# Kernel tuning notes

Hardware: AMD Instinct MI355X
Metric: run time of the kernel (lower is better)

## Reference

```python
import jax, jax.numpy as jnp
import numpy as np
from jax import lax
import math

N_QUBITS = 10
N_LAYERS = 4
PI = jnp.float32(math.pi)


def _c(x):
    return x.astype(jnp.complex64)


def rx_mat(t):
    c = _c(jnp.cos(0.5 * t)); s = _c(jnp.sin(0.5 * t))
    return jnp.stack([jnp.stack([c, -1j * s]), jnp.stack([-1j * s, c])])


def ry_mat(t):
    c = _c(jnp.cos(0.5 * t)); s = _c(jnp.sin(0.5 * t))
    return jnp.stack([jnp.stack([c, -s]), jnp.stack([s, c])])


def rz_mat(t):
    e0 = jnp.exp(_c(jnp.zeros_like(t)) - 0.5j * _c(t))
    e1 = jnp.exp(0.5j * _c(t))
    z = jnp.zeros_like(e0)
    return jnp.stack([jnp.stack([e0, z]), jnp.stack([z, e1])])


def apply_1q(psi, U, q):
    # psi: (2,)*n complex, apply 2x2 U on axis q
    psi = jnp.moveaxis(psi, q, 0)
    psi = jnp.tensordot(U, psi, axes=(1, 0))
    return jnp.moveaxis(psi, 0, q)


def apply_cnot(psi, ctrl, tgt):
    psi = jnp.moveaxis(psi, (ctrl, tgt), (0, 1))
    a00, a01, a10, a11 = psi[0, 0], psi[0, 1], psi[1, 0], psi[1, 1]
    psi = jnp.stack([jnp.stack([a00, a01]), jnp.stack([a11, a10])])
    return jnp.moveaxis(psi, (0, 1), (ctrl, tgt))


def vqc(state, weights):
    # state: (D,) float32 angles; weights: (layers, n, 3)
    n, L = N_QUBITS, N_LAYERS
    D = state.shape[0]
    psi = jnp.full((2,) * n, 2.0 ** (-n / 2.0), dtype=jnp.complex64)  # H^n |0>
    for layer in range(L):
        for q in range(n):
            ang = state[(layer * n + q) % D]
            psi = apply_1q(psi, rx_mat(ang), q)
            psi = apply_1q(psi, ry_mat(ang), q)
            psi = apply_1q(psi, rz_mat(weights[layer, q, 0]), q)
            psi = apply_1q(psi, ry_mat(weights[layer, q, 1]), q)
            psi = apply_1q(psi, rz_mat(weights[layer, q, 2]), q)
        for q in range(n - 1):
            psi = apply_cnot(psi, q, q + 1)
        psi = apply_cnot(psi, n - 1, 0)
    probs = jnp.real(psi * jnp.conj(psi))  # (2,)*n
    zdiag = jnp.array([1.0, -1.0], dtype=jnp.float32)
    exps = [jnp.sum(probs * zdiag.reshape((1,) * q + (2,) + (1,) * (n - q - 1)))
            for q in range(n)]
    return jnp.stack(exps)  # (n,)


def lstm_forward(x, W_ih, W_hh, b_ih, b_hh):
    # x: [B,T,Din]; PyTorch gate order: i, f, g, o
    B, T, _ = x.shape
    H = W_hh.shape[1]
    b = b_ih + b_hh

    def step(carry, xt):
        h, c = carry
        gates = xt @ W_ih.T + h @ W_hh.T + b
        i, f, g, o = jnp.split(gates, 4, axis=-1)
        i = jax.nn.sigmoid(i); f = jax.nn.sigmoid(f)
        g = jnp.tanh(g); o = jax.nn.sigmoid(o)
        c = f * c + i * g
        h = o * jnp.tanh(c)
        return (h, c), h

    h0 = jnp.zeros((B, H), x.dtype)
    c0 = jnp.zeros((B, H), x.dtype)
    _, hs = lax.scan(step, (h0, c0), jnp.swapaxes(x, 0, 1))
    return jnp.swapaxes(hs, 0, 1)  # [B,T,H]


def _forward(s, lstm_s, W_ih, W_hh, b_ih, b_hh, proj_W, proj_b,
             in_proj_W, in_proj_b, out_proj_W, out_proj_b,
             qweights, W1, b1, W2, b2):
    hs = lstm_forward(lstm_s, W_ih, W_hh, b_ih, b_hh)      # [B,T,H]
    lstm_last = hs[:, -1, :]                               # [B,H]
    state_full = jnp.concatenate([lstm_last, s], axis=1)   # [B,E]
    lstm_proj = hs @ proj_W.T + proj_b                     # [B,T,E]
    E = proj_W.shape[0]
    Wq, Wk, Wv = in_proj_W[:E], in_proj_W[E:2 * E], in_proj_W[2 * E:]
    bq, bk, bv = in_proj_b[:E], in_proj_b[E:2 * E], in_proj_b[2 * E:]
    q = state_full @ Wq.T + bq                             # [B,E] (1 query token)
    k = lstm_proj @ Wk.T + bk                              # [B,T,E]
    v = lstm_proj @ Wv.T + bv
    scale = 1.0 / jnp.sqrt(jnp.float32(E))                 # num_heads=1 -> head_dim=E
    attn = jax.nn.softmax(jnp.einsum('be,bte->bt', q, k) * scale, axis=-1)
    ctx = jnp.einsum('bt,bte->be', attn, v)
    attn_out = ctx @ out_proj_W.T + out_proj_b             # [B,E]
    merged_state = jnp.concatenate([attn_out, s], axis=1)  # [B,E+F]
    state_norm = jnp.tanh(merged_state) * PI
    qfeat = jax.vmap(lambda st: vqc(st, qweights))(state_norm)  # [B,n]
    merged = jnp.concatenate([merged_state, qfeat], axis=1)
    x = jax.nn.relu(merged @ W1.T + b1)
    return x @ W2.T + b2


def setup_inputs() -> dict:
    key = jax.random.key(0)
    ks = jax.random.split(key, 16)
    B, T = 512, 256
    Din, H, F = 128, 256, 64
    E = H + F          # 320 = state_dim
    Dm = E + F         # 384 = merged_state dim
    n_l1, n_act = 512, 8

    def g(k, shape, std):
        return (std * jax.random.normal(k, shape)).astype(jnp.float32)

    return {
        's': jax.random.normal(ks[0], (B, F), jnp.float32),
        'lstm_s': jax.random.normal(ks[1], (B, T, Din), jnp.float32),
        'W_ih': g(ks[2], (4 * H, Din), 0.05),
        'W_hh': g(ks[3], (4 * H, H), 0.05),
        'b_ih': jnp.zeros((4 * H,), jnp.float32),
        'b_hh': jnp.zeros((4 * H,), jnp.float32),
        'proj_W': g(ks[4], (E, H), 0.05),
        'proj_b': 0.1 * jnp.ones((E,), jnp.float32),
        'in_proj_W': g(ks[5], (3 * E, E), 0.05),
        'in_proj_b': jnp.zeros((3 * E,), jnp.float32),
        'out_proj_W': g(ks[6], (E, E), 0.05),
        'out_proj_b': jnp.zeros((E,), jnp.float32),
        'qweights': jax.random.uniform(ks[7], (N_LAYERS, N_QUBITS, 3), jnp.float32, 0.0, 2.0 * math.pi),
        'W1': g(ks[8], (n_l1, Dm + N_QUBITS), 0.05),
        'b1': 0.1 * jnp.ones((n_l1,), jnp.float32),
        'W2': g(ks[9], (n_act, n_l1), 0.05),
        'b2': 0.1 * jnp.ones((n_act,), jnp.float32),
    }


def reference(s, lstm_s, W_ih, W_hh, b_ih, b_hh, proj_W, proj_b,
              in_proj_W, in_proj_b, out_proj_W, out_proj_b,
              qweights, W1, b1, W2, b2):
    return _forward(s, lstm_s, W_ih, W_hh, b_ih, b_hh, proj_W, proj_b,
                    in_proj_W, in_proj_b, out_proj_W, out_proj_b,
                    qweights, W1, b1, W2, b2)
```

## Files before the change

### kernel.cpp

```cpp
#include <hip/hip_runtime.h>
#include <hip/hip_bf16.h>
#include <math.h>

typedef unsigned int u32;
typedef unsigned long long u64;
typedef unsigned short u16;
typedef __attribute__((ext_vector_type(8))) short short8;
typedef __attribute__((ext_vector_type(4))) float f32x4;
typedef __attribute__((ext_vector_type(4))) int v4i;

#define PI_F 3.14159265358979f
#define B_   512
#define T_   256
#define DIN  128
#define H_   256
#define G4   1024
#define F_   64
#define E_   320
#define DM   384
#define NL1  512
#define NACT 8
#define KMLP 394

__device__ v4i llvm_amdgcn_raw_buffer_load_v4i32(v4i rsrc, int voffset,
                                                 int soffset, int aux)
    __asm("llvm.amdgcn.raw.buffer.load.v4i32");
__device__ void llvm_amdgcn_raw_buffer_store_i32(int vdata, v4i rsrc,
                                                 int voffset, int soffset,
                                                 int aux)
    __asm("llvm.amdgcn.raw.buffer.store.i32");

__device__ __forceinline__ v4i make_srd(const void* p) {
  v4i r;
  r.x = (int)(u32)(u64)p;
  r.y = (int)(u32)((u64)p >> 32);
  r.z = (int)0xFFFFFFFFu;
  r.w = 0x00020000;
  return r;
}

__device__ __forceinline__ float b2f(u16 h) {
  union { u32 u; float f; } v; v.u = ((u32)h) << 16; return v.f;
}
__device__ __forceinline__ u16 f2b(float f) {
  union { float f; u32 u; } v; v.f = f;
  u32 r = (v.u + 0x7FFFu + ((v.u >> 16) & 1u)) >> 16;
  return (u16)r;
}
__device__ __forceinline__ float sigf(float x) { return 1.0f / (1.0f + __expf(-x)); }
__device__ __forceinline__ float tanhfast(float x) { return 2.0f / (1.0f + __expf(-2.0f * x)) - 1.0f; }
__device__ __forceinline__ float2 cmul(float2 a, float2 b) {
  return make_float2(a.x * b.x - a.y * b.y, a.x * b.y + a.y * b.x);
}
__device__ __forceinline__ float2 cadd(float2 a, float2 b) {
  return make_float2(a.x + b.x, a.y + b.y);
}

__global__ void k_prep1(const float* __restrict__ lstm_s,
                        const float* __restrict__ W_ih,
                        const float* __restrict__ W_hh,
                        const float* __restrict__ b_ih,
                        const float* __restrict__ b_hh,
                        const float* __restrict__ ipw,
                        const float* __restrict__ ipb,
                        const float* __restrict__ projb,
                        const float* __restrict__ qw,
                        const float* __restrict__ W1,
                        u16* __restrict__ xbf,
                        u16* __restrict__ hs,
                        u16* __restrict__ Wg,
                        float* __restrict__ bb,
                        float* __restrict__ W1t,
                        float* __restrict__ uw,
                        float* __restrict__ bkp,
                        float* __restrict__ bvp,
                        u32* __restrict__ cnt) {
  const int bid = blockIdx.x;
  const int tid = threadIdx.x;
  if (bid < 8192) {
    u32 u = (u32)bid * 256u + tid;
    u32 c8 = u & 15u, b = (u >> 4) & 511u, t = u >> 13;
    const float* src = lstm_s + ((size_t)b * T_ + t) * DIN + c8 * 8;
    union { u16 h[8]; uint4 v; } tmp;
#pragma unroll
    for (int i = 0; i < 8; ++i) tmp.h[i] = f2b(src[i]);
    *(uint4*)(xbf + ((size_t)t * B_ + b) * DIN + c8 * 8) = tmp.v;
  } else if (bid < 8384) {
    u32 u = (u32)(bid - 8192) * 256u + tid;
    u32 c8 = u % 48u, r = u / 48u;
    const float* src = (c8 < 16) ? (W_ih + (size_t)r * DIN + c8 * 8)
                                 : (W_hh + (size_t)r * H_ + (c8 - 16) * 8);
    union { u16 h[8]; uint4 v; } tmp;
#pragma unroll
    for (int i = 0; i < 8; ++i) tmp.h[i] = f2b(src[i]);
    *(uint4*)(Wg + (size_t)r * 384 + c8 * 8) = tmp.v;
  } else if (bid < 8448) {
    u32 u = (u32)(bid - 8384) * 256u + tid;
    ((uint4*)hs)[u] = make_uint4(0, 0, 0, 0);
  } else if (bid < 9236) {
    u32 u = (u32)(bid - 8448) * 256u + tid;
    u32 k = u / 512u, nn = u % 512u;
    W1t[u] = W1[(size_t)nn * KMLP + k];
  } else if (bid == 9236) {
    for (int i = tid; i < 1024; i += 256) bb[i] = b_ih[i] + b_hh[i];
    for (int i = tid; i < 1024; i += 256) cnt[i] = 0u;
    if (tid < 40) {
      float w0 = qw[tid * 3 + 0], w1 = qw[tid * 3 + 1], w2 = qw[tid * 3 + 2];
      float c0 = cosf(0.5f * w0), s0 = sinf(0.5f * w0);
      float c1 = cosf(0.5f * w1), s1 = sinf(0.5f * w1);
      float c2 = cosf(0.5f * w2), s2 = sinf(0.5f * w2);
      float2 e0m = make_float2(c0, -s0), e0p = make_float2(c0, s0);
      float2 e2m = make_float2(c2, -s2), e2p = make_float2(c2, s2);
      float2 t00 = make_float2(c1 * e0m.x, c1 * e0m.y);
      float2 t01 = make_float2(-s1 * e0p.x, -s1 * e0p.y);
      float2 t10 = make_float2(s1 * e0m.x, s1 * e0m.y);
      float2 t11 = make_float2(c1 * e0p.x, c1 * e0p.y);
      float2 u00 = cmul(e2m, t00), u01 = cmul(e2m, t01);
      float2 u10 = cmul(e2p, t10), u11 = cmul(e2p, t11);
      float* o = uw + tid * 8;
      o[0] = u00.x; o[1] = u00.y; o[2] = u01.x; o[3] = u01.y;
      o[4] = u10.x; o[5] = u10.y; o[6] = u11.x; o[7] = u11.y;
    }
  } else if (bid <= 9238) {
    int o = (bid - 9237) * 256 + tid;
    if (o < E_) {
      float acc = ipb[E_ + o];
      for (int e = 0; e < E_; ++e) acc += ipw[(size_t)(E_ + o) * E_ + e] * projb[e];
      bkp[o] = acc;
    }
  } else {
    int o = (bid - 9239) * 256 + tid;
    if (o < E_) {
      float acc = ipb[2 * E_ + o];
      for (int e = 0; e < E_; ++e) acc += ipw[(size_t)(2 * E_ + o) * E_ + e] * projb[e];
      bvp[o] = acc;
    }
  }
}

__global__ void k_prep2(const float* __restrict__ ipw, const float* __restrict__ projW,
                        float* __restrict__ Wkp, float* __restrict__ Wvp) {
  int bid = blockIdx.x, tid = threadIdx.x;
  int o = (bid < 320) ? bid : (bid - 320);
  const float* wrow = ipw + (size_t)((bid < 320 ? E_ : 2 * E_) + o) * E_;
  float acc = 0.f;
  for (int e = 0; e < E_; ++e) acc += wrow[e] * projW[(size_t)e * H_ + tid];
  (bid < 320 ? Wkp : Wvp)[(size_t)o * H_ + tid] = acc;
}

__global__ void k_prep3(const float* __restrict__ ipw, const float* __restrict__ ipb,
                        const float* __restrict__ opw, const float* __restrict__ opb,
                        const float* __restrict__ Wkp, const float* __restrict__ Wvp,
                        const float* __restrict__ bkp, const float* __restrict__ bvp,
                        float* __restrict__ WuT, float* __restrict__ bu,
                        float* __restrict__ wd, float* __restrict__ ddp,
                        float* __restrict__ Wovt, float* __restrict__ bov) {
  int bid = blockIdx.x, tid = threadIdx.x;
  if (bid < 320) {
    int e = bid;
    float acc = 0.f;
    for (int o = 0; o < E_; ++o) acc += Wkp[(size_t)o * H_ + tid] * ipw[(size_t)o * E_ + e];
    WuT[(size_t)e * H_ + tid] = acc;
  } else if (bid < 576) {
    int jj = bid - 320;
    for (int i = tid; i < E_; i += 256) {
      float acc = 0.f;
      for (int o = 0; o < E_; ++o) acc += opw[(size_t)i * E_ + o] * Wvp[(size_t)o * H_ + jj];
      Wovt[(size_t)jj * E_ + i] = acc;
    }
  } else {
    {
      float acc = 0.f;
      for (int o = 0; o < E_; ++o) acc += Wkp[(size_t)o * H_ + tid] * ipb[o];
      bu[tid] = acc;
    }
    for (int idx = tid; idx < E_; idx += 256) {
      float a1 = 0.f, a2 = opb[idx];
      for (int o = 0; o < E_; ++o) {
        a1 += ipw[(size_t)o * E_ + idx] * bkp[o];
        a2 += opw[(size_t)idx * E_ + o] * bvp[o];
      }
      wd[idx] = a1; bov[idx] = a2;
    }
    if (tid == 0) {
      float acc = 0.f;
      for (int o = 0; o < E_; ++o) acc += ipb[o] * bkp[o];
      ddp[0] = acc;
    }
  }
}

struct LstmArgs {
  const u16* xbf; u16* hs; const u16* Wg; const float* bb; u32* cnt;
};

__launch_bounds__(256, 1)
__global__ void k_lstm(LstmArgs A) {
  const int g   = blockIdx.x & 7;
  const int n   = blockIdx.x >> 3;
  const int tid = threadIdx.x;
  const int wid = tid >> 6, lane = tid & 63;
  __shared__ __align__(16) u16 Wl[32 * 392];

  for (int idx = tid; idx < 32 * 48; idx += 256) {
    int ln = idx / 48, c8 = idx % 48;
    int gr = (ln >> 3) * 256 + n * 8 + (ln & 7);
    *(uint4*)&Wl[ln * 392 + c8 * 8] = *(const uint4*)&A.Wg[(size_t)gr * 384 + c8 * 8];
  }
  const int j  = lane & 7;
  const int gc = n * 8 + j;
  const float bbi = A.bb[gc], bbf2 = A.bb[256 + gc];
  const float bbg = A.bb[512 + gc], bbo = A.bb[768 + gc];

  const int quad = lane >> 4;
  const int mrow = lane & 15;
  const int brow = g * 64 + wid * 16 + mrow;
  const int erow0 = g * 64 + wid * 16 + quad * 4;
  const bool hi = (lane & 8) != 0;
  float crs[4] = {0.f, 0.f, 0.f, 0.f};
  u32* mycnt = A.cnt + g * 64;
  u32 target = 0;

  const v4i hs_srd = make_srd(A.hs);
  const int hvoff = (brow * H_ + quad * 8) * 2;

  uint4 xc0, xc1, xc2, xc3, xn0, xn1, xn2, xn3;
  {
    const u16* xb = A.xbf + ((size_t)0 * B_ + brow) * DIN + quad * 8;
    xc0 = *(const uint4*)(xb + 0);
    xc1 = *(const uint4*)(xb + 32);
    xc2 = *(const uint4*)(xb + 64);
    xc3 = *(const uint4*)(xb + 96);
  }
  __syncthreads();

  for (int t = 0; t < T_; ++t) {
    const int hsoff = t * (B_ * H_ * 2);
    uint4 h0 = __builtin_bit_cast(uint4, llvm_amdgcn_raw_buffer_load_v4i32(hs_srd, hvoff +   0, hsoff, 17));
    uint4 h1 = __builtin_bit_cast(uint4, llvm_amdgcn_raw_buffer_load_v4i32(hs_srd, hvoff +  64, hsoff, 17));
    uint4 h2 = __builtin_bit_cast(uint4, llvm_amdgcn_raw_buffer_load_v4i32(hs_srd, hvoff + 128, hsoff, 17));
    uint4 h3 = __builtin_bit_cast(uint4, llvm_amdgcn_raw_buffer_load_v4i32(hs_srd, hvoff + 192, hsoff, 17));
    uint4 h4 = __builtin_bit_cast(uint4, llvm_amdgcn_raw_buffer_load_v4i32(hs_srd, hvoff + 256, hsoff, 17));
    uint4 h5 = __builtin_bit_cast(uint4, llvm_amdgcn_raw_buffer_load_v4i32(hs_srd, hvoff + 320, hsoff, 17));
    uint4 h6 = __builtin_bit_cast(uint4, llvm_amdgcn_raw_buffer_load_v4i32(hs_srd, hvoff + 384, hsoff, 17));
    uint4 h7 = __builtin_bit_cast(uint4, llvm_amdgcn_raw_buffer_load_v4i32(hs_srd, hvoff + 448, hsoff, 17));
    {
      const int tn = (t + 1 < T_) ? (t + 1) : t;
      const u16* xb = A.xbf + ((size_t)tn * B_ + brow) * DIN + quad * 8;
      xn0 = *(const uint4*)(xb + 0);
      xn1 = *(const uint4*)(xb + 32);
      xn2 = *(const uint4*)(xb + 64);
      xn3 = *(const uint4*)(xb + 96);
    }

    f32x4 acc0 = {0.f, 0.f, 0.f, 0.f}, acc1 = {0.f, 0.f, 0.f, 0.f};
#define MMSTEP(AV, KOFF)                                                          \
    {                                                                             \
      short8 av  = __builtin_bit_cast(short8, AV);                                \
      short8 bv0 = __builtin_bit_cast(short8,                                     \
          *(const uint4*)&Wl[mrow * 392 + (KOFF) + quad * 8]);                    \
      short8 bv1 = __builtin_bit_cast(short8,                                     \
          *(const uint4*)&Wl[(16 + mrow) * 392 + (KOFF) + quad * 8]);             \
      acc0 = __builtin_amdgcn_mfma_f32_16x16x32_bf16(av, bv0, acc0, 0, 0, 0);     \
      acc1 = __builtin_amdgcn_mfma_f32_16x16x32_bf16(av, bv1, acc1, 0, 0, 0);     \
    }
    MMSTEP(xc0, 0)   MMSTEP(xc1, 32)  MMSTEP(xc2, 64)  MMSTEP(xc3, 96)
    MMSTEP(h0, 128)  MMSTEP(h1, 160)  MMSTEP(h2, 192)  MMSTEP(h3, 224)
    MMSTEP(h4, 256)  MMSTEP(h5, 288)  MMSTEP(h6, 320)  MMSTEP(h7, 352)
#undef MMSTEP

    const int hsoff_o = (t + 1) * (B_ * H_ * 2);
#pragma unroll
    for (int r = 0; r < 4; ++r) {
      float x0 = acc0[r], x1v = acc1[r];
      float y0 = __shfl_xor(x0, 8, 64);
      float y1 = __shfl_xor(x1v, 8, 64);
      float iv = (hi ? y0 : x0) + bbi;
      float fv = (hi ? x0 : y0) + bbf2;
      float gv = (hi ? y1 : x1v) + bbg;
      float ov = (hi ? x1v : y1) + bbo;
      float cc = sigf(fv) * crs[r] + sigf(iv) * tanhfast(gv);
      crs[r] = cc;
      float hh = sigf(ov) * tanhfast(cc);
      float hh2 = __shfl_xor(hh, 1, 64);
      if (!hi && ((j & 1) == 0)) {
        u32 pk = (u32)f2b(hh) | ((u32)f2b(hh2) << 16);
        llvm_amdgcn_raw_buffer_store_i32((int)pk, hs_srd,
                                         ((erow0 + r) * H_ + gc) * 2, hsoff_o, 17);
      }
    }
    target += 32;
    if (t != T_ - 1) {
      __syncthreads();
      if (tid == 0) {
        __hip_atomic_fetch_add(mycnt, 1u, __ATOMIC_RELAXED, __HIP_MEMORY_SCOPE_AGENT);
        int guard = 0;
        while (__hip_atomic_load(mycnt, __ATOMIC_RELAXED, __HIP_MEMORY_SCOPE_AGENT) < target) {
          __builtin_amdgcn_s_sleep(1);
          if (++guard > (1 << 24)) break;
        }
      }
      __syncthreads();
      xc0 = xn0; xc1 = xn1; xc2 = xn2; xc3 = xn3;
    }
  }
}

__global__ void k_u(const u16* __restrict__ hs, const float* __restrict__ s,
                    const float* __restrict__ WuT, const float* __restrict__ bu,
                    const float* __restrict__ wd, const float* __restrict__ ddp,
                    float* __restrict__ u, float* __restrict__ dvec) {
  int b = blockIdx.x, tid = threadIdx.x;
  __shared__ float z[E_];
  __shared__ float red[256];
  z[tid] = b2f(hs[((size_t)T_ * B_ + b) * H_ + tid]);
  if (tid < F_) z[H_ + tid] = s[(size_t)b * F_ + tid];
  __syncthreads();
  float acc = bu[tid];
  for (int e = 0; e < E_; ++e) acc += WuT[(size_t)e * H_ + tid] * z[e];
  u[(size_t)b * H_ + tid] = acc;
  float p = 0.f;
  for (int e = tid; e < E_; e += 256) p += wd[e] * z[e];
  red[tid] = p;
  __syncthreads();
  for (int s2 = 128; s2 > 0; s2 >>= 1) {
    if (tid < s2) red[tid] += red[tid + s2];
    __syncthreads();
  }
  if (tid == 0) dvec[b] = red[0] + ddp[0];
}

__global__ void k_aw(const u16* __restrict__ hs, const float* __restrict__ u,
                     const float* __restrict__ dvec, float* __restrict__ wv) {
  int b = blockIdx.x, tid = threadIdx.x;
  int wid = tid >> 6, lane = tid & 63;
  __shared__ float sc[T_];
  __shared__ float red[256];
  const float db = dvec[b];
  const float scale = 0.055901699437494745f;
  float4 ul = *(const float4*)&u[(size_t)b * H_ + lane * 4];
  for (int tt = 0; tt < 64; ++tt) {
    int t = wid * 64 + tt;
    u32 rw0 = ((const u32*)(hs + ((size_t)(t + 1) * B_ + b) * H_))[lane * 2];
    u32 rw1 = ((const u32*)(hs + ((size_t)(t + 1) * B_ + b) * H_))[lane * 2 + 1];
    union { u32 uu; float f; } f0, f1, f2, f3;
    f0.uu = rw0 << 16; f1.uu = rw0 & 0xFFFF0000u;
    f2.uu = rw1 << 16; f3.uu = rw1 & 0xFFFF0000u;
    float p = f0.f * ul.x + f1.f * ul.y + f2.f * ul.z + f3.f * ul.w;
#pragma unroll
    for (int off = 32; off > 0; off >>= 1) p += __shfl_xor(p, off, 64);
    if (lane == 0) sc[t] = (p + db) * scale;
  }
  __syncthreads();
  float v = sc[tid];
  red[tid] = v;
  __syncthreads();
  for (int s2 = 128; s2 > 0; s2 >>= 1) {
    if (tid < s2) red[tid] = fmaxf(red[tid], red[tid + s2]);
    __syncthreads();
  }
  float m = red[0];
  __syncthreads();
  float e = __expf(v - m);
  red[tid] = e;
  __syncthreads();
  for (int s2 = 128; s2 > 0; s2 >>= 1) {
    if (tid < s2) red[tid] += red[tid + s2];
    __syncthreads();
  }
  float inv = 1.f / red[0];
  __syncthreads();
  sc[tid] = e * inv;
  __syncthreads();
  float acc = 0.f;
#pragma unroll 8
  for (int t = 0; t < T_; ++t) {
    acc += sc[t] * b2f(hs[((size_t)(t + 1) * B_ + b) * H_ + tid]);
  }
  wv[(size_t)b * H_ + tid] = acc;
}

__global__ void k_ao(const float* __restrict__ wv, const float* __restrict__ Wovt,
                     const float* __restrict__ bov, const float* __restrict__ s,
                     float* __restrict__ mst) {
  int b = blockIdx.x, tid = threadIdx.x;
  __shared__ float wl[H_];
  if (tid < H_) wl[tid] = wv[(size_t)b * H_ + tid];
  __syncthreads();
  if (tid < E_) {
    float acc = bov[tid];
    for (int jj = 0; jj < H_; ++jj) acc += Wovt[(size_t)jj * E_ + tid] * wl[jj];
    mst[(size_t)b * DM + tid] = acc;
  } else if (tid < DM) {
    mst[(size_t)b * DM + tid] = s[(size_t)b * F_ + (tid - E_)];
  }
}

__global__ void k_vqc(const float* __restrict__ mst, const float* __restrict__ uwg,
                      float* __restrict__ qf) {
  int b = blockIdx.x, tid = threadIdx.x;
  __shared__ float2 psi[1024];
  __shared__ float ang[40];
  __shared__ float uwl[320];
  __shared__ float part[4][10];
  if (tid < 40) ang[tid] = tanhf(mst[(size_t)b * DM + tid]) * PI_F;
  uwl[tid] = uwg[tid];
  if (tid < 64) uwl[256 + tid] = uwg[256 + tid];
#pragma unroll
  for (int k = 0; k < 4; ++k) psi[tid + k * 256] = make_float2(0.03125f, 0.f);
  __syncthreads();
  for (int l = 0; l < 4; ++l) {
    for (int q = 0; q < 10; ++q) {
      int lq = l * 10 + q;
      float a = ang[lq];
      float ca = __cosf(0.5f * a), sa = __sinf(0.5f * a);
      float cs = ca * sa;
      float2 m00 = make_float2(ca * ca, sa * sa);
      float2 m01 = make_float2(-cs, -cs);
      float2 m10 = make_float2(cs, -cs);
      float2 m11 = make_float2(ca * ca, -sa * sa);
      const float* uwp = &uwl[lq * 8];
      float2 a00 = make_float2(uwp[0], uwp[1]), a01 = make_float2(uwp[2], uwp[3]);
      float2 a10 = make_float2(uwp[4], uwp[5]), a11 = make_float2(uwp[6], uwp[7]);
      float2 u00 = cadd(cmul(a00, m00), cmul(a01, m10));
      float2 u01 = cadd(cmul(a00, m01), cmul(a01, m11));
      float2 u10 = cadd(cmul(a10, m00), cmul(a11, m10));
      float2 u11 = cadd(cmul(a10, m01), cmul(a11, m11));
      int bp = 9 - q;
      __syncthreads();
#pragma unroll
      for (int k = 0; k < 2; ++k) {
        int p = tid + k * 256;
        int i0 = ((p >> bp) << (bp + 1)) | (p & ((1 << bp) - 1));
        int i1 = i0 | (1 << bp);
        float2 A0 = psi[i0], A1 = psi[i1];
        psi[i0] = cadd(cmul(u00, A0), cmul(u01, A1));
        psi[i1] = cadd(cmul(u10, A0), cmul(u11, A1));
      }
    }
    for (int q = 0; q < 9; ++q) {
      int lo = 8 - q;
      __syncthreads();
      int p = tid;
      int i0 = ((p >> lo) << (lo + 2)) | (2 << lo) | (p & ((1 << lo) - 1));
      int i1 = i0 | (1 << lo);
      float2 tmp = psi[i0]; psi[i0] = psi[i1]; psi[i1] = tmp;
    }
    __syncthreads();
    {
      int i0 = (tid << 1) | 1;
      int i1 = i0 | 512;
      float2 tmp = psi[i0]; psi[i0] = psi[i1]; psi[i1] = tmp;
    }
  }
  __syncthreads();
  float acc[10];
#pragma unroll
  for (int q = 0; q < 10; ++q) acc[q] = 0.f;
#pragma unroll
  for (int k = 0; k < 4; ++k) {
    int idx = tid + k * 256;
    float2 A = psi[idx];
    float pr = A.x * A.x + A.y * A.y;
#pragma unroll
    for (int q = 0; q < 10; ++q) acc[q] += ((idx >> (9 - q)) & 1) ? -pr : pr;
  }
  int lane = tid & 63, wid = tid >> 6;
#pragma unroll
  for (int q = 0; q < 10; ++q) {
    float vq = acc[q];
#pragma unroll
    for (int off = 32; off > 0; off >>= 1) vq += __shfl_xor(vq, off, 64);
    if (lane == 0) part[wid][q] = vq;
  }
  __syncthreads();
  if (tid < 10) qf[(size_t)b * 10 + tid] = part[0][tid] + part[1][tid] + part[2][tid] + part[3][tid];
}

__global__ void k_mlp(const float* __restrict__ mst, const float* __restrict__ qf,
                      const float* __restrict__ W1t, const float* __restrict__ b1,
                      const float* __restrict__ W2, const float* __restrict__ b2,
                      float* __restrict__ out) {
  int b = blockIdx.x, tid = threadIdx.x;
  __shared__ float mg[KMLP];
  __shared__ float x1[NL1];
  __shared__ float red[256];
  for (int i = tid; i < DM; i += 256) mg[i] = mst[(size_t)b * DM + i];
  if (tid < 10) mg[DM + tid] = qf[(size_t)b * 10 + tid];
  __syncthreads();
#pragma unroll
  for (int hh = 0; hh < 2; ++hh) {
    int nn = tid + hh * 256;
    float acc = b1[nn];
#pragma unroll 4
    for (int k = 0; k < KMLP; ++k) acc += W1t[(size_t)k * NL1 + nn] * mg[k];
    x1[nn] = fmaxf(acc, 0.f);
  }
  __syncthreads();
  int a = tid >> 5, l32 = tid & 31;
  float p = 0.f;
  for (int k = l32; k < NL1; k += 32) p += x1[k] * W2[(size_t)a * NL1 + k];
  red[tid] = p;
  __syncthreads();
  if (tid < 8) {
    float acc = b2[tid];
#pragma unroll
    for (int i = 0; i < 32; ++i) acc += red[tid * 32 + i];
    out[(size_t)b * NACT + tid] = acc;
  }
}

extern "C" void kernel_launch(void* const* d_in, const int* in_sizes, int n_in,
                              void* d_out, int out_size, void* d_ws, size_t ws_size,
                              hipStream_t stream) {
  const float* s      = (const float*)d_in[0];
  const float* lstm_s = (const float*)d_in[1];
  const float* W_ih   = (const float*)d_in[2];
  const float* W_hh   = (const float*)d_in[3];
  const float* b_ih   = (const float*)d_in[4];
  const float* b_hh   = (const float*)d_in[5];
  const float* projW  = (const float*)d_in[6];
  const float* projb  = (const float*)d_in[7];
  const float* ipw    = (const float*)d_in[8];
  const float* ipb    = (const float*)d_in[9];
  const float* opw    = (const float*)d_in[10];
  const float* opb    = (const float*)d_in[11];
  const float* qw     = (const float*)d_in[12];
  const float* W1     = (const float*)d_in[13];
  const float* b1     = (const float*)d_in[14];
  const float* W2     = (const float*)d_in[15];
  const float* b2     = (const float*)d_in[16];
  float* out = (float*)d_out;

  char* wsb = (char*)d_ws;
  size_t off = 0;
  auto alloc = [&](size_t bytes) -> void* {
    void* p = wsb + off;
    off = (off + bytes + 255) & ~(size_t)255;
    return p;
  };
  u16*  xbf  = (u16*)alloc((size_t)T_ * B_ * DIN * 2);
  u16*  hs   = (u16*)alloc((size_t)(T_ + 1) * B_ * H_ * 2);
  u16*  Wg   = (u16*)alloc((size_t)G4 * 384 * 2);
  float* bb  = (float*)alloc(G4 * 4);
  float* Wkp = (float*)alloc((size_t)E_ * H_ * 4);
  float* Wvp = (float*)alloc((size_t)E_ * H_ * 4);
  float* bkp = (float*)alloc(E_ * 4);
  float* bvp = (float*)alloc(E_ * 4);
  float* WuT = (float*)alloc((size_t)E_ * H_ * 4);
  float* bu  = (float*)alloc(H_ * 4);
  float* wd  = (float*)alloc(E_ * 4);
  float* ddp = (float*)alloc(256);
  float* Wovt= (float*)alloc((size_t)H_ * E_ * 4);
  float* bov = (float*)alloc(E_ * 4);
  float* uu  = (float*)alloc((size_t)B_ * H_ * 4);
  float* dvec= (float*)alloc(B_ * 4);
  float* wv  = (float*)alloc((size_t)B_ * H_ * 4);
  float* mst = (float*)alloc((size_t)B_ * DM * 4);
  float* qf  = (float*)alloc((size_t)B_ * 10 * 4);
  float* uw  = (float*)alloc(40 * 8 * 4);
  float* W1t = (float*)alloc((size_t)KMLP * NL1 * 4);
  u32*  cnt  = (u32*)alloc(1024 * 4);
  (void)ws_size; (void)in_sizes; (void)n_in; (void)out_size;

  hipLaunchKernelGGL(k_prep1, dim3(9241), dim3(256), 0, stream,
                     lstm_s, W_ih, W_hh, b_ih, b_hh, ipw, ipb, projb, qw, W1,
                     xbf, hs, Wg, bb, W1t, uw, bkp, bvp, cnt);
  hipLaunchKernelGGL(k_prep2, dim3(640), dim3(256), 0, stream, ipw, projW, Wkp, Wvp);
  hipLaunchKernelGGL(k_prep3, dim3(577), dim3(256), 0, stream,
                     ipw, ipb, opw, opb, Wkp, Wvp, bkp, bvp, WuT, bu, wd, ddp, Wovt, bov);

  LstmArgs la;
  la.xbf = xbf; la.hs = hs; la.Wg = Wg; la.bb = bb; la.cnt = cnt;
  void* kargs[] = { (void*)&la };
  hipError_t ce = hipLaunchCooperativeKernel(reinterpret_cast<const void*>(&k_lstm),
                                             dim3(256), dim3(256), kargs, 0, stream);
  if (ce != hipSuccess) {
    hipLaunchKernelGGL(k_lstm, dim3(256), dim3(256), 0, stream, la);
  }

  hipLaunchKernelGGL(k_u,   dim3(512), dim3(256), 0, stream, hs, s, WuT, bu, wd, ddp, uu, dvec);
  hipLaunchKernelGGL(k_aw,  dim3(512), dim3(256), 0, stream, hs, uu, dvec, wv);
  hipLaunchKernelGGL(k_ao,  dim3(512), dim3(384), 0, stream, wv, Wovt, bov, s, mst);
  hipLaunchKernelGGL(k_vqc, dim3(512), dim3(256), 0, stream, mst, uw, qf);
  hipLaunchKernelGGL(k_mlp, dim3(512), dim3(256), 0, stream, mst, qf, W1t, b1, W2, b2, out);
}
```

Before: 1.333 ms.

## Replace LSTM counter barrier with sentinel-polling dataflow sync and wider per-block tiles

The LSTM kernel drops the per-step atomic counter barrier between blocks. Instead, the hidden-state buffer for steps 1..T is pre-filled with a bf16 sentinel pattern, and each wave polls its own h loads until no sentinel remains. Blocks now compute 32 hidden columns (all four gates) instead of 8, and the grid shrinks from 256 to 64 blocks. The recurrent weights are held in registers and the input weights stay in LDS. The aim is to cut barrier latency and weight reloads, at the cost of heavy register pressure and a large sentinel-fill pass in the prep kernel. Correctness relies on a computed bf16 value never equaling the sentinel (-inf) and on visibility of the stores to other blocks.

Result: slower. 1.994 ms (+49.6%).

```diff
diff --git a/kernel.cpp b/kernel.cpp
--- a/kernel.cpp
+++ b/kernel.cpp
@@ -55,6 +55,8 @@
 __device__ __forceinline__ float2 cadd(float2 a, float2 b) {
   return make_float2(a.x + b.x, a.y + b.y);
 }
+
+#define SENT 0xFF80FF80u
 
 __global__ void k_prep1(const float* __restrict__ lstm_s,
                         const float* __restrict__ W_ih,
@@ -128,13 +130,17 @@
       for (int e = 0; e < E_; ++e) acc += ipw[(size_t)(E_ + o) * E_ + e] * projb[e];
       bkp[o] = acc;
     }
-  } else {
+  } else if (bid <= 9240) {
     int o = (bid - 9239) * 256 + tid;
     if (o < E_) {
       float acc = ipb[2 * E_ + o];
       for (int e = 0; e < E_; ++e) acc += ipw[(size_t)(2 * E_ + o) * E_ + e] * projb[e];
       bvp[o] = acc;
     }
+  } else {
+    u32 u = (u32)(bid - 9241) * 256u + tid;
+    ((uint4*)(hs + (size_t)B_ * H_))[u] =
+        make_uint4(SENT, SENT, SENT, SENT);
   }
 }
 
@@ -200,29 +206,42 @@
   const int n   = blockIdx.x >> 3;
   const int tid = threadIdx.x;
   const int wid = tid >> 6, lane = tid & 63;
-  __shared__ __align__(16) u16 Wl[32 * 392];
-
-  for (int idx = tid; idx < 32 * 48; idx += 256) {
-    int ln = idx / 48, c8 = idx % 48;
-    int gr = (ln >> 3) * 256 + n * 8 + (ln & 7);
-    *(uint4*)&Wl[ln * 392 + c8 * 8] = *(const uint4*)&A.Wg[(size_t)gr * 384 + c8 * 8];
-  }
-  const int j  = lane & 7;
-  const int gc = n * 8 + j;
-  const float bbi = A.bb[gc], bbf2 = A.bb[256 + gc];
-  const float bbg = A.bb[512 + gc], bbo = A.bb[768 + gc];
-
   const int quad = lane >> 4;
   const int mrow = lane & 15;
+  __shared__ __align__(16) u16 Wlx[128 * 136];
+
+  for (int idx = tid; idx < 128 * 16; idx += 256) {
+    int ln = idx >> 4, c8 = idx & 15;
+    int gr = (ln >> 5) * 256 + n * 32 + (ln & 31);
+    *(uint4*)&Wlx[ln * 136 + c8 * 8] = *(const uint4*)&A.Wg[(size_t)gr * 384 + c8 * 8];
+  }
+
+  short8 WB[8][8];
+#pragma unroll
+  for (int b = 0; b < 8; ++b) {
+    const int br = b * 16 + mrow;
+    const int gr = (br >> 5) * 256 + n * 32 + (br & 31);
+    const u16* wp = A.Wg + (size_t)gr * 384 + 128 + quad * 8;
+#pragma unroll
+    for (int kc = 0; kc < 8; ++kc)
+      WB[b][kc] = *(const short8*)(wp + kc * 32);
+  }
+
+  float bbv[2][4];
+#pragma unroll
+  for (int half = 0; half < 2; ++half) {
+    const int c = n * 32 + half * 16 + mrow;
+    bbv[half][0] = A.bb[c];
+    bbv[half][1] = A.bb[256 + c];
+    bbv[half][2] = A.bb[512 + c];
+    bbv[half][3] = A.bb[768 + c];
+  }
+
   const int brow = g * 64 + wid * 16 + mrow;
-  const int erow0 = g * 64 + wid * 16 + quad * 4;
-  const bool hi = (lane & 8) != 0;
-  float crs[4] = {0.f, 0.f, 0.f, 0.f};
-  u32* mycnt = A.cnt + g * 64;
-  u32 target = 0;
-
+  float crs[2][4] = {{0.f, 0.f, 0.f, 0.f}, {0.f, 0.f, 0.f, 0.f}};
   const v4i hs_srd = make_srd(A.hs);
   const int hvoff = (brow * H_ + quad * 8) * 2;
+  const int so_base = ((g * 64 + wid * 16 + quad * 4) * H_ + n * 32 + mrow) * 2;
 
   uint4 xc0, xc1, xc2, xc3, xn0, xn1, xn2, xn3;
   {
@@ -234,16 +253,52 @@
   }
   __syncthreads();
 
+#define LOADH()                                                                                          \
+    h0 = __builtin_bit_cast(uint4, llvm_amdgcn_raw_buffer_load_v4i32(hs_srd, hvoff +   0, hsoff, 17));   \
+    h1 = __builtin_bit_cast(uint4, llvm_amdgcn_raw_buffer_load_v4i32(hs_srd, hvoff +  64, hsoff, 17));   \
+    h2 = __builtin_bit_cast(uint4, llvm_amdgcn_raw_buffer_load_v4i32(hs_srd, hvoff + 128, hsoff, 17));   \
+    h3 = __builtin_bit_cast(uint4, llvm_amdgcn_raw_buffer_load_v4i32(hs_srd, hvoff + 192, hsoff, 17));   \
+    h4 = __builtin_bit_cast(uint4, llvm_amdgcn_raw_buffer_load_v4i32(hs_srd, hvoff + 256, hsoff, 17));   \
+    h5 = __builtin_bit_cast(uint4, llvm_amdgcn_raw_buffer_load_v4i32(hs_srd, hvoff + 320, hsoff, 17));   \
+    h6 = __builtin_bit_cast(uint4, llvm_amdgcn_raw_buffer_load_v4i32(hs_srd, hvoff + 384, hsoff, 17));   \
+    h7 = __builtin_bit_cast(uint4, llvm_amdgcn_raw_buffer_load_v4i32(hs_srd, hvoff + 448, hsoff, 17));
+
+#define CHK4(v) (((v).x == SENT) | ((v).y == SENT) | ((v).z == SENT) | ((v).w == SENT))
+
+#define LDSB(b, kc) __builtin_bit_cast(short8,                                        \
+    *(const uint4*)&Wlx[((b) * 16 + mrow) * 136 + (kc) * 32 + quad * 8])
+
+#define XSTEP(XV, KC)                                                                 \
+    {                                                                                 \
+      short8 av = __builtin_bit_cast(short8, XV);                                     \
+      acc0 = __builtin_amdgcn_mfma_f32_16x16x32_bf16(av, LDSB(0, KC), acc0, 0, 0, 0); \
+      acc1 = __builtin_amdgcn_mfma_f32_16x16x32_bf16(av, LDSB(1, KC), acc1, 0, 0, 0); \
+      acc2 = __builtin_amdgcn_mfma_f32_16x16x32_bf16(av, LDSB(2, KC), acc2, 0, 0, 0); \
+      acc3 = __builtin_amdgcn_mfma_f32_16x16x32_bf16(av, LDSB(3, KC), acc3, 0, 0, 0); \
+      acc4 = __builtin_amdgcn_mfma_f32_16x16x32_bf16(av, LDSB(4, KC), acc4, 0, 0, 0); \
+      acc5 = __builtin_amdgcn_mfma_f32_16x16x32_bf16(av, LDSB(5, KC), acc5, 0, 0, 0); \
+      acc6 = __builtin_amdgcn_mfma_f32_16x16x32_bf16(av, LDSB(6, KC), acc6, 0, 0, 0); \
+      acc7 = __builtin_amdgcn_mfma_f32_16x16x32_bf16(av, LDSB(7, KC), acc7, 0, 0, 0); \
+    }
+
+#define HSTEP(HV, KC)                                                                   \
+    {                                                                                   \
+      short8 av = __builtin_bit_cast(short8, HV);                                       \
+      acc0 = __builtin_amdgcn_mfma_f32_16x16x32_bf16(av, WB[0][KC], acc0, 0, 0, 0);     \
+      acc1 = __builtin_amdgcn_mfma_f32_16x16x32_bf16(av, WB[1][KC], acc1, 0, 0, 0);     \
+      acc2 = __builtin_amdgcn_mfma_f32_16x16x32_bf16(av, WB[2][KC], acc2, 0, 0, 0);     \
+      acc3 = __builtin_amdgcn_mfma_f32_16x16x32_bf16(av, WB[3][KC], acc3, 0, 0, 0);     \
+      acc4 = __builtin_amdgcn_mfma_f32_16x16x32_bf16(av, WB[4][KC], acc4, 0, 0, 0);     \
+      acc5 = __builtin_amdgcn_mfma_f32_16x16x32_bf16(av, WB[5][KC], acc5, 0, 0, 0);     \
+      acc6 = __builtin_amdgcn_mfma_f32_16x16x32_bf16(av, WB[6][KC], acc6, 0, 0, 0);     \
+      acc7 = __builtin_amdgcn_mfma_f32_16x16x32_bf16(av, WB[7][KC], acc7, 0, 0, 0);     \
+    }
+
   for (int t = 0; t < T_; ++t) {
     const int hsoff = t * (B_ * H_ * 2);
-    uint4 h0 = __builtin_bit_cast(uint4, llvm_amdgcn_raw_buffer_load_v4i32(hs_srd, hvoff +   0, hsoff, 17));
-    uint4 h1 = __builtin_bit_cast(uint4, llvm_amdgcn_raw_buffer_load_v4i32(hs_srd, hvoff +  64, hsoff, 17));
-    uint4 h2 = __builtin_bit_cast(uint4, llvm_amdgcn_raw_buffer_load_v4i32(hs_srd, hvoff + 128, hsoff, 17));
-    uint4 h3 = __builtin_bit_cast(uint4, llvm_amdgcn_raw_buffer_load_v4i32(hs_srd, hvoff + 192, hsoff, 17));
-    uint4 h4 = __builtin_bit_cast(uint4, llvm_amdgcn_raw_buffer_load_v4i32(hs_srd, hvoff + 256, hsoff, 17));
-    uint4 h5 = __builtin_bit_cast(uint4, llvm_amdgcn_raw_buffer_load_v4i32(hs_srd, hvoff + 320, hsoff, 17));
-    uint4 h6 = __builtin_bit_cast(uint4, llvm_amdgcn_raw_buffer_load_v4i32(hs_srd, hvoff + 384, hsoff, 17));
-    uint4 h7 = __builtin_bit_cast(uint4, llvm_amdgcn_raw_buffer_load_v4i32(hs_srd, hvoff + 448, hsoff, 17));
+    uint4 h0, h1, h2, h3, h4, h5, h6, h7;
+    LOADH();
+
     {
       const int tn = (t + 1 < T_) ? (t + 1) : t;
       const u16* xb = A.xbf + ((size_t)tn * B_ + brow) * DIN + quad * 8;
@@ -254,56 +309,67 @@
     }
 
     f32x4 acc0 = {0.f, 0.f, 0.f, 0.f}, acc1 = {0.f, 0.f, 0.f, 0.f};
-#define MMSTEP(AV, KOFF)                                                          \
-    {                                                                             \
-      short8 av  = __builtin_bit_cast(short8, AV);                                \
-      short8 bv0 = __builtin_bit_cast(short8,                                     \
-          *(const uint4*)&Wl[mrow * 392 + (KOFF) + quad * 8]);                    \
-      short8 bv1 = __builtin_bit_cast(short8,                                     \
-          *(const uint4*)&Wl[(16 + mrow) * 392 + (KOFF) + quad * 8]);             \
-      acc0 = __builtin_amdgcn_mfma_f32_16x16x32_bf16(av, bv0, acc0, 0, 0, 0);     \
-      acc1 = __builtin_amdgcn_mfma_f32_16x16x32_bf16(av, bv1, acc1, 0, 0, 0);     \
-    }
-    MMSTEP(xc0, 0)   MMSTEP(xc1, 32)  MMSTEP(xc2, 64)  MMSTEP(xc3, 96)
-    MMSTEP(h0, 128)  MMSTEP(h1, 160)  MMSTEP(h2, 192)  MMSTEP(h3, 224)
-    MMSTEP(h4, 256)  MMSTEP(h5, 288)  MMSTEP(h6, 320)  MMSTEP(h7, 352)
-#undef MMSTEP
-
-    const int hsoff_o = (t + 1) * (B_ * H_ * 2);
+    f32x4 acc2 = {0.f, 0.f, 0.f, 0.f}, acc3 = {0.f, 0.f, 0.f, 0.f};
+    f32x4 acc4 = {0.f, 0.f, 0.f, 0.f}, acc5 = {0.f, 0.f, 0.f, 0.f};
+    f32x4 acc6 = {0.f, 0.f, 0.f, 0.f}, acc7 = {0.f, 0.f, 0.f, 0.f};
+
+    XSTEP(xc0, 0) XSTEP(xc1, 1) XSTEP(xc2, 2) XSTEP(xc3, 3)
+
+    {
+      int guard = 0;
+      while (__any((int)(CHK4(h0) | CHK4(h1) | CHK4(h2) | CHK4(h3) |
+                         CHK4(h4) | CHK4(h5) | CHK4(h6) | CHK4(h7)))) {
+        if (++guard > (1 << 18)) break;
+        __builtin_amdgcn_s_sleep(1);
+        asm volatile("" ::: "memory");
+        LOADH();
+      }
+    }
+
+    HSTEP(h0, 0) HSTEP(h1, 1) HSTEP(h2, 2) HSTEP(h3, 3)
+    HSTEP(h4, 4) HSTEP(h5, 5) HSTEP(h6, 6) HSTEP(h7, 7)
+
+    const int hsoff_o = hsoff + (B_ * H_ * 2);
 #pragma unroll
     for (int r = 0; r < 4; ++r) {
-      float x0 = acc0[r], x1v = acc1[r];
-      float y0 = __shfl_xor(x0, 8, 64);
-      float y1 = __shfl_xor(x1v, 8, 64);
-      float iv = (hi ? y0 : x0) + bbi;
-      float fv = (hi ? x0 : y0) + bbf2;
-      float gv = (hi ? y1 : x1v) + bbg;
-      float ov = (hi ? x1v : y1) + bbo;
-      float cc = sigf(fv) * crs[r] + sigf(iv) * tanhfast(gv);
-      crs[r] = cc;
-      float hh = sigf(ov) * tanhfast(cc);
-      float hh2 = __shfl_xor(hh, 1, 64);
-      if (!hi && ((j & 1) == 0)) {
-        u32 pk = (u32)f2b(hh) | ((u32)f2b(hh2) << 16);
-        llvm_amdgcn_raw_buffer_store_i32((int)pk, hs_srd,
-                                         ((erow0 + r) * H_ + gc) * 2, hsoff_o, 17);
-      }
-    }
-    target += 32;
-    if (t != T_ - 1) {
-      __syncthreads();
-      if (tid == 0) {
-        __hip_atomic_fetch_add(mycnt, 1u, __ATOMIC_RELAXED, __HIP_MEMORY_SCOPE_AGENT);
-        int guard = 0;
-        while (__hip_atomic_load(mycnt, __ATOMIC_RELAXED, __HIP_MEMORY_SCOPE_AGENT) < target) {
-          __builtin_amdgcn_s_sleep(1);
-          if (++guard > (1 << 24)) break;
+      {
+        float iv = acc0[r] + bbv[0][0];
+        float fv = acc2[r] + bbv[0][1];
+        float gv = acc4[r] + bbv[0][2];
+        float ov = acc6[r] + bbv[0][3];
+        float cc = sigf(fv) * crs[0][r] + sigf(iv) * tanhfast(gv);
+        crs[0][r] = cc;
+        float hh = sigf(ov) * tanhfast(cc);
+        float hh2 = __shfl_xor(hh, 1, 64);
+        if ((lane & 1) == 0) {
+          u32 pk = (u32)f2b(hh) | ((u32)f2b(hh2) << 16);
+          llvm_amdgcn_raw_buffer_store_i32((int)pk, hs_srd,
+                                           so_base + r * (H_ * 2), hsoff_o, 17);
         }
       }
-      __syncthreads();
-      xc0 = xn0; xc1 = xn1; xc2 = xn2; xc3 = xn3;
-    }
-  }
+      {
+        float iv = acc1[r] + bbv[1][0];
+        float fv = acc3[r] + bbv[1][1];
+        float gv = acc5[r] + bbv[1][2];
+        float ov = acc7[r] + bbv[1][3];
+        float cc = sigf(fv) * crs[1][r] + sigf(iv) * tanhfast(gv);
+        crs[1][r] = cc;
+        float hh = sigf(ov) * tanhfast(cc);
+        float hh2 = __shfl_xor(hh, 1, 64);
+        if ((lane & 1) == 0) {
+          u32 pk = (u32)f2b(hh) | ((u32)f2b(hh2) << 16);
+          llvm_amdgcn_raw_buffer_store_i32((int)pk, hs_srd,
+                                           so_base + r * (H_ * 2) + 32, hsoff_o, 17);
+        }
+      }
+    }
+    xc0 = xn0; xc1 = xn1; xc2 = xn2; xc3 = xn3;
+  }
+#undef LOADH
+#undef CHK4
+#undef LDSB
+#undef XSTEP
+#undef HSTEP
 }
 
 __global__ void k_u(const u16* __restrict__ hs, const float* __restrict__ s,
@@ -563,7 +629,7 @@
   u32*  cnt  = (u32*)alloc(1024 * 4);
   (void)ws_size; (void)in_sizes; (void)n_in; (void)out_size;
 
-  hipLaunchKernelGGL(k_prep1, dim3(9241), dim3(256), 0, stream,
+  hipLaunchKernelGGL(k_prep1, dim3(25625), dim3(256), 0, stream,
                      lstm_s, W_ih, W_hh, b_ih, b_hh, ipw, ipb, projb, qw, W1,
                      xbf, hs, Wg, bb, W1t, uw, bkp, bvp, cnt);
   hipLaunchKernelGGL(k_prep2, dim3(640), dim3(256), 0, stream, ipw, projW, Wkp, Wvp);
@@ -574,9 +640,9 @@
   la.xbf = xbf; la.hs = hs; la.Wg = Wg; la.bb = bb; la.cnt = cnt;
   void* kargs[] = { (void*)&la };
   hipError_t ce = hipLaunchCooperativeKernel(reinterpret_cast<const void*>(&k_lstm),
-                                             dim3(256), dim3(256), kargs, 0, stream);
+                                             dim3(64), dim3(256), kargs, 0, stream);
   if (ce != hipSuccess) {
-    hipLaunchKernelGGL(k_lstm, dim3(256), dim3(256), 0, stream, la);
+    hipLaunchKernelGGL(k_lstm, dim3(64), dim3(256), 0, stream, la);
   }
 
   hipLaunchKernelGGL(k_u,   dim3(512), dim3(256), 0, stream, hs, s, WuT, bu, wd, ddp, uu, dvec);
```

## Replace per-step LSTM group barrier with sentinel-based dataflow polling on hidden states

Applied to the files above, without the earlier changes.

The per-timestep group counter barrier (syncthreads, atomic add, spin, syncthreads) in the persistent LSTM kernel is removed. Instead, the hidden-state buffer for steps 1..T is pre-filled with a NaN-like bf16 sentinel in the prep kernel, and each wave spins per 16-byte chunk until the sentinel is overwritten by the producer. This lets waves consume h as soon as each piece arrives rather than waiting for the whole group barrier. The cost is an extra fill of about 64 MB of hs memory, plus reliance on the sentinel never appearing as a real value and on store visibility without explicit fences.

Result: slower. 3.213 ms (+141.0%).

```diff
diff --git a/kernel.cpp b/kernel.cpp
--- a/kernel.cpp
+++ b/kernel.cpp
@@ -55,6 +55,8 @@
 __device__ __forceinline__ float2 cadd(float2 a, float2 b) {
   return make_float2(a.x + b.x, a.y + b.y);
 }
+
+#define SENT 0xFF80FF80u
 
 __global__ void k_prep1(const float* __restrict__ lstm_s,
                         const float* __restrict__ W_ih,
@@ -128,13 +130,17 @@
       for (int e = 0; e < E_; ++e) acc += ipw[(size_t)(E_ + o) * E_ + e] * projb[e];
       bkp[o] = acc;
     }
-  } else {
+  } else if (bid <= 9240) {
     int o = (bid - 9239) * 256 + tid;
     if (o < E_) {
       float acc = ipb[2 * E_ + o];
       for (int e = 0; e < E_; ++e) acc += ipw[(size_t)(2 * E_ + o) * E_ + e] * projb[e];
       bvp[o] = acc;
     }
+  } else {
+    u32 u = (u32)(bid - 9241) * 256u + tid;
+    ((uint4*)(hs + (size_t)B_ * H_))[u] =
+        make_uint4(SENT, SENT, SENT, SENT);
   }
 }
 
@@ -218,8 +224,6 @@
   const int erow0 = g * 64 + wid * 16 + quad * 4;
   const bool hi = (lane & 8) != 0;
   float crs[4] = {0.f, 0.f, 0.f, 0.f};
-  u32* mycnt = A.cnt + g * 64;
-  u32 target = 0;
 
   const v4i hs_srd = make_srd(A.hs);
   const int hvoff = (brow * H_ + quad * 8) * 2;
@@ -233,6 +237,31 @@
     xc3 = *(const uint4*)(xb + 96);
   }
   __syncthreads();
+
+#define CHK4(v) (((v).x == SENT) | ((v).y == SENT) | ((v).z == SENT) | ((v).w == SENT))
+
+#define WAITCHUNK(HK, OFF)                                                            \
+    {                                                                                 \
+      int gd = 0;                                                                     \
+      while (__any((int)CHK4(HK))) {                                                  \
+        if (++gd > (1 << 22)) break;                                                  \
+        __builtin_amdgcn_s_sleep(1);                                                  \
+        asm volatile("" ::: "memory");                                                \
+        HK = __builtin_bit_cast(uint4,                                                \
+            llvm_amdgcn_raw_buffer_load_v4i32(hs_srd, hvoff + (OFF), hsoff, 17));     \
+      }                                                                               \
+    }
+
+#define MMSTEP(AV, KOFF)                                                          \
+    {                                                                             \
+      short8 av  = __builtin_bit_cast(short8, AV);                                \
+      short8 bv0 = __builtin_bit_cast(short8,                                     \
+          *(const uint4*)&Wl[mrow * 392 + (KOFF) + quad * 8]);                    \
+      short8 bv1 = __builtin_bit_cast(short8,                                     \
+          *(const uint4*)&Wl[(16 + mrow) * 392 + (KOFF) + quad * 8]);             \
+      acc0 = __builtin_amdgcn_mfma_f32_16x16x32_bf16(av, bv0, acc0, 0, 0, 0);     \
+      acc1 = __builtin_amdgcn_mfma_f32_16x16x32_bf16(av, bv1, acc1, 0, 0, 0);     \
+    }
 
   for (int t = 0; t < T_; ++t) {
     const int hsoff = t * (B_ * H_ * 2);
@@ -254,22 +283,17 @@
     }
 
     f32x4 acc0 = {0.f, 0.f, 0.f, 0.f}, acc1 = {0.f, 0.f, 0.f, 0.f};
-#define MMSTEP(AV, KOFF)                                                          \
-    {                                                                             \
-      short8 av  = __builtin_bit_cast(short8, AV);                                \
-      short8 bv0 = __builtin_bit_cast(short8,                                     \
-          *(const uint4*)&Wl[mrow * 392 + (KOFF) + quad * 8]);                    \
-      short8 bv1 = __builtin_bit_cast(short8,                                     \
-          *(const uint4*)&Wl[(16 + mrow) * 392 + (KOFF) + quad * 8]);             \
-      acc0 = __builtin_amdgcn_mfma_f32_16x16x32_bf16(av, bv0, acc0, 0, 0, 0);     \
-      acc1 = __builtin_amdgcn_mfma_f32_16x16x32_bf16(av, bv1, acc1, 0, 0, 0);     \
-    }
     MMSTEP(xc0, 0)   MMSTEP(xc1, 32)  MMSTEP(xc2, 64)  MMSTEP(xc3, 96)
-    MMSTEP(h0, 128)  MMSTEP(h1, 160)  MMSTEP(h2, 192)  MMSTEP(h3, 224)
-    MMSTEP(h4, 256)  MMSTEP(h5, 288)  MMSTEP(h6, 320)  MMSTEP(h7, 352)
-#undef MMSTEP
-
-    const int hsoff_o = (t + 1) * (B_ * H_ * 2);
+    WAITCHUNK(h0,   0)  MMSTEP(h0, 128)
+    WAITCHUNK(h1,  64)  MMSTEP(h1, 160)
+    WAITCHUNK(h2, 128)  MMSTEP(h2, 192)
+    WAITCHUNK(h3, 192)  MMSTEP(h3, 224)
+    WAITCHUNK(h4, 256)  MMSTEP(h4, 256)
+    WAITCHUNK(h5, 320)  MMSTEP(h5, 288)
+    WAITCHUNK(h6, 384)  MMSTEP(h6, 320)
+    WAITCHUNK(h7, 448)  MMSTEP(h7, 352)
+
+    const int hsoff_o = hsoff + (B_ * H_ * 2);
 #pragma unroll
     for (int r = 0; r < 4; ++r) {
       float x0 = acc0[r], x1v = acc1[r];
@@ -289,21 +313,11 @@
                                          ((erow0 + r) * H_ + gc) * 2, hsoff_o, 17);
       }
     }
-    target += 32;
-    if (t != T_ - 1) {
-      __syncthreads();
-      if (tid == 0) {
-        __hip_atomic_fetch_add(mycnt, 1u, __ATOMIC_RELAXED, __HIP_MEMORY_SCOPE_AGENT);
-        int guard = 0;
-        while (__hip_atomic_load(mycnt, __ATOMIC_RELAXED, __HIP_MEMORY_SCOPE_AGENT) < target) {
-          __builtin_amdgcn_s_sleep(1);
-          if (++guard > (1 << 24)) break;
-        }
-      }
-      __syncthreads();
-      xc0 = xn0; xc1 = xn1; xc2 = xn2; xc3 = xn3;
-    }
-  }
+    xc0 = xn0; xc1 = xn1; xc2 = xn2; xc3 = xn3;
+  }
+#undef CHK4
+#undef WAITCHUNK
+#undef MMSTEP
 }
 
 __global__ void k_u(const u16* __restrict__ hs, const float* __restrict__ s,
@@ -563,7 +577,7 @@
   u32*  cnt  = (u32*)alloc(1024 * 4);
   (void)ws_size; (void)in_sizes; (void)n_in; (void)out_size;
 
-  hipLaunchKernelGGL(k_prep1, dim3(9241), dim3(256), 0, stream,
+  hipLaunchKernelGGL(k_prep1, dim3(25625), dim3(256), 0, stream,
                      lstm_s, W_ih, W_hh, b_ih, b_hh, ipw, ipb, projb, qw, W1,
                      xbf, hs, Wg, bb, W1t, uw, bkp, bvp, cnt);
   hipLaunchKernelGGL(k_prep2, dim3(640), dim3(256), 0, stream, ipw, projW, Wkp, Wvp);
```

## Replace block-level atomic counter barrier with per-wave flag arrays in LSTM recurrence

Applied to the files above, without the earlier changes.

The per-timestep group barrier, which used __syncthreads plus a single thread doing an atomic add and spinning on a shared counter, is replaced with per-wave flag stores into a per-timestep flag array. Each wave writes its own flag after draining its stores and polls the 32 producer flags it depends on with a vector buffer load and ballot. This removes the intra-block __syncthreads pair and serialized atomic contention from the critical path of each recurrence step. It costs a larger zeroed flag buffer (T×4×8×32 words) and extra prep blocks to clear it, and memory ordering now relies on the vmcnt wait and uncached buffer accesses.

Result: slower. 1.924 ms (+44.3%).

```diff
diff --git a/kernel.cpp b/kernel.cpp
--- a/kernel.cpp
+++ b/kernel.cpp
@@ -103,7 +103,6 @@
     W1t[u] = W1[(size_t)nn * KMLP + k];
   } else if (bid == 9236) {
     for (int i = tid; i < 1024; i += 256) bb[i] = b_ih[i] + b_hh[i];
-    for (int i = tid; i < 1024; i += 256) cnt[i] = 0u;
     if (tid < 40) {
       float w0 = qw[tid * 3 + 0], w1 = qw[tid * 3 + 1], w2 = qw[tid * 3 + 2];
       float c0 = cosf(0.5f * w0), s0 = sinf(0.5f * w0);
@@ -128,13 +127,16 @@
       for (int e = 0; e < E_; ++e) acc += ipw[(size_t)(E_ + o) * E_ + e] * projb[e];
       bkp[o] = acc;
     }
-  } else {
+  } else if (bid <= 9240) {
     int o = (bid - 9239) * 256 + tid;
     if (o < E_) {
       float acc = ipb[2 * E_ + o];
       for (int e = 0; e < E_; ++e) acc += ipw[(size_t)(2 * E_ + o) * E_ + e] * projb[e];
       bvp[o] = acc;
     }
+  } else {
+    u32 u = (u32)(bid - 9241) * 256u + tid;
+    ((uint4*)cnt)[u] = make_uint4(0, 0, 0, 0);
   }
 }
 
@@ -218,11 +220,12 @@
   const int erow0 = g * 64 + wid * 16 + quad * 4;
   const bool hi = (lane & 8) != 0;
   float crs[4] = {0.f, 0.f, 0.f, 0.f};
-  u32* mycnt = A.cnt + g * 64;
-  u32 target = 0;
 
   const v4i hs_srd = make_srd(A.hs);
+  const v4i fl_srd = make_srd(A.cnt);
   const int hvoff = (brow * H_ + quad * 8) * 2;
+  const int fl_row0 = ((wid * 8 + g) * 32) * 4;
+  const int fl_lane = (lane & 7) * 16;
 
   uint4 xc0, xc1, xc2, xc3, xn0, xn1, xn2, xn3;
   {
@@ -233,6 +236,17 @@
     xc3 = *(const uint4*)(xb + 96);
   }
   __syncthreads();
+
+#define MMSTEP(AV, KOFF)                                                          \
+    {                                                                             \
+      short8 av  = __builtin_bit_cast(short8, AV);                                \
+      short8 bv0 = __builtin_bit_cast(short8,                                     \
+          *(const uint4*)&Wl[mrow * 392 + (KOFF) + quad * 8]);                    \
+      short8 bv1 = __builtin_bit_cast(short8,                                     \
+          *(const uint4*)&Wl[(16 + mrow) * 392 + (KOFF) + quad * 8]);             \
+      acc0 = __builtin_amdgcn_mfma_f32_16x16x32_bf16(av, bv0, acc0, 0, 0, 0);     \
+      acc1 = __builtin_amdgcn_mfma_f32_16x16x32_bf16(av, bv1, acc1, 0, 0, 0);     \
+    }
 
   for (int t = 0; t < T_; ++t) {
     const int hsoff = t * (B_ * H_ * 2);
@@ -254,22 +268,11 @@
     }
 
     f32x4 acc0 = {0.f, 0.f, 0.f, 0.f}, acc1 = {0.f, 0.f, 0.f, 0.f};
-#define MMSTEP(AV, KOFF)                                                          \
-    {                                                                             \
-      short8 av  = __builtin_bit_cast(short8, AV);                                \
-      short8 bv0 = __builtin_bit_cast(short8,                                     \
-          *(const uint4*)&Wl[mrow * 392 + (KOFF) + quad * 8]);                    \
-      short8 bv1 = __builtin_bit_cast(short8,                                     \
-          *(const uint4*)&Wl[(16 + mrow) * 392 + (KOFF) + quad * 8]);             \
-      acc0 = __builtin_amdgcn_mfma_f32_16x16x32_bf16(av, bv0, acc0, 0, 0, 0);     \
-      acc1 = __builtin_amdgcn_mfma_f32_16x16x32_bf16(av, bv1, acc1, 0, 0, 0);     \
-    }
     MMSTEP(xc0, 0)   MMSTEP(xc1, 32)  MMSTEP(xc2, 64)  MMSTEP(xc3, 96)
     MMSTEP(h0, 128)  MMSTEP(h1, 160)  MMSTEP(h2, 192)  MMSTEP(h3, 224)
     MMSTEP(h4, 256)  MMSTEP(h5, 288)  MMSTEP(h6, 320)  MMSTEP(h7, 352)
-#undef MMSTEP
-
-    const int hsoff_o = (t + 1) * (B_ * H_ * 2);
+
+    const int hsoff_o = hsoff + (B_ * H_ * 2);
 #pragma unroll
     for (int r = 0; r < 4; ++r) {
       float x0 = acc0[r], x1v = acc1[r];
@@ -289,21 +292,28 @@
                                          ((erow0 + r) * H_ + gc) * 2, hsoff_o, 17);
       }
     }
-    target += 32;
+
     if (t != T_ - 1) {
-      __syncthreads();
-      if (tid == 0) {
-        __hip_atomic_fetch_add(mycnt, 1u, __ATOMIC_RELAXED, __HIP_MEMORY_SCOPE_AGENT);
-        int guard = 0;
-        while (__hip_atomic_load(mycnt, __ATOMIC_RELAXED, __HIP_MEMORY_SCOPE_AGENT) < target) {
+      asm volatile("s_waitcnt vmcnt(0)" ::: "memory");
+      const int frow = t * 4096 + fl_row0;
+      if (lane == 0) {
+        llvm_amdgcn_raw_buffer_store_i32(1, fl_srd, frow + n * 4, 0, 17);
+      }
+      {
+        int gd = 0;
+        while (true) {
+          v4i f = llvm_amdgcn_raw_buffer_load_v4i32(fl_srd, frow + fl_lane, 0, 17);
+          bool ok = (f.x != 0) && (f.y != 0) && (f.z != 0) && (f.w != 0);
+          if (__ballot(ok) == ~0ull) break;
+          if (++gd > (1 << 22)) break;
           __builtin_amdgcn_s_sleep(1);
-          if (++guard > (1 << 24)) break;
+          asm volatile("" ::: "memory");
         }
       }
-      __syncthreads();
-      xc0 = xn0; xc1 = xn1; xc2 = xn2; xc3 = xn3;
-    }
-  }
+    }
+    xc0 = xn0; xc1 = xn1; xc2 = xn2; xc3 = xn3;
+  }
+#undef MMSTEP
 }
 
 __global__ void k_u(const u16* __restrict__ hs, const float* __restrict__ s,
@@ -560,10 +570,10 @@
   float* qf  = (float*)alloc((size_t)B_ * 10 * 4);
   float* uw  = (float*)alloc(40 * 8 * 4);
   float* W1t = (float*)alloc((size_t)KMLP * NL1 * 4);
-  u32*  cnt  = (u32*)alloc(1024 * 4);
+  u32*  cnt  = (u32*)alloc((size_t)T_ * 4 * 8 * 32 * 4);
   (void)ws_size; (void)in_sizes; (void)n_in; (void)out_size;
 
-  hipLaunchKernelGGL(k_prep1, dim3(9241), dim3(256), 0, stream,
+  hipLaunchKernelGGL(k_prep1, dim3(9497), dim3(256), 0, stream,
                      lstm_s, W_ih, W_hh, b_ih, b_hh, ipw, ipb, projb, qw, W1,
                      xbf, hs, Wg, bb, W1t, uw, bkp, bvp, cnt);
   hipLaunchKernelGGL(k_prep2, dim3(640), dim3(256), 0, stream, ipw, projW, Wkp, Wvp);
```
